# Optimization experiments

Measured on AMD Instinct MI355X. Metric: run time of the kernel, lower is better.

## Reference

```python
import jax, jax.numpy as jnp
import numpy as np

SOM_H, SOM_W = 16, 16
K = SOM_H * SOM_W          # num_embeddings = 256
EMB_D = 32                 # embedding_dim
ALPHA, BETA = 6.0, 1.0


def _build_tables():
    """Static SOM grid neighbor tables (rectangular geometry).
    ind[k] is a 0/1 row over the K codebook entries marking k and its
    up/down/left/right grid neighbors; counts[k] = number of neighbors incl self.
    Replaces the original per-voxel Python loop with a constant lookup table.
    """
    ind = np.zeros((K, K), np.float32)
    for idx in range(K):
        h, w = divmod(idx, SOM_W)
        neigh = [idx]
        if h - 1 >= 0:
            neigh.append((h - 1) * SOM_W + w)
        if h + 1 < SOM_H:
            neigh.append((h + 1) * SOM_W + w)
        if w - 1 >= 0:
            neigh.append(h * SOM_W + (w - 1))
        if w + 1 < SOM_W:
            neigh.append(h * SOM_W + (w + 1))
        ind[idx, neigh] = 1.0
    counts = ind.sum(axis=1)
    return jnp.asarray(ind), jnp.asarray(counts)

_IND_TABLE, _COUNTS = _build_tables()


def setup_inputs() -> dict:
    key = jax.random.key(0)
    k1, k2 = jax.random.split(key)
    x = jax.random.normal(k1, (8, EMB_D, 32, 32, 32), dtype=jnp.float32)  # [B,C,D,H,W]
    W = jax.random.normal(k2, (K, EMB_D), dtype=jnp.float32)              # codebook
    return {"x": x, "W": W}


def reference(x, W):
    # channels-last: [B, D, H, Wd, C]
    inputs = jnp.transpose(x, (0, 2, 3, 4, 1))
    in_shape = inputs.shape
    flat = inputs.reshape(-1, EMB_D)                    # [N, d]
    flat_sg = jax.lax.stop_gradient(flat)               # matches flat_inputs.detach()

    # squared Euclidean distances to all codebook entries: [N, K]
    dist = (jnp.sum(flat_sg ** 2, axis=1, keepdims=True)
            + jnp.sum(W ** 2, axis=1)
            - 2.0 * flat_sg @ W.T)

    enc_idx = jnp.argmin(dist, axis=1)                  # [N]
    encodings = jax.nn.one_hot(enc_idx, K, dtype=inputs.dtype)  # [N, K]

    quantized = (encodings @ W).reshape(in_shape)
    commitment_loss = jnp.mean((quantized - inputs) ** 2)

    # vectorized neighbor indicator + counts via static table gather
    indicator = _IND_TABLE[enc_idx]                     # [N, K], constant wrt floats
    total_neighbors = jnp.sum(_COUNTS[enc_idx])
    somloss = jnp.sum(dist * indicator) / total_neighbors

    loss = ALPHA * commitment_loss + BETA * somloss

    # straight-through estimator
    quantized_st = inputs + jax.lax.stop_gradient(quantized - inputs)
    out = jnp.transpose(quantized_st, (0, 4, 1, 2, 3))  # back to [B,C,D,H,W]
    return loss, out, encodings
```

## Files before the change

kernel.cpp:

```cpp
#include <hip/hip_runtime.h>


#define SOM_K      256
#define EMB_D      32
#define WPAD       36
#define N_VOX      262144
#define SPATIAL    32768
#define OUT_ELEMS  8388608
#define COMMIT_DEN 8388608.0f
#define NSLOT      256

__global__ __launch_bounds__(256) void som_prep_kernel(float* __restrict__ ws) {
  float4* p = (float4*)ws;
  int t = threadIdx.x;
#pragma unroll
  for (int i = 0; i < 4; ++i) p[i * 256 + t] = make_float4(0.f, 0.f, 0.f, 0.f);
}

__global__ __launch_bounds__(256) void som_main_kernel(
    const float* __restrict__ x,
    const float* __restrict__ w,
    float* __restrict__ slots,
    float* __restrict__ out,
    float* __restrict__ enc) {
  __shared__ __align__(16) float wl[SOM_K * WPAD];
  __shared__ float wsql[SOM_K];

  const int t = threadIdx.x;

  const int n    = blockIdx.x * 256 + t;
  const int base = (n >> 15) * (EMB_D * SPATIAL) + (n & (SPATIAL - 1));
  float xv[EMB_D];
#pragma unroll
  for (int c = 0; c < EMB_D; ++c) xv[c] = x[base + c * SPATIAL];

#pragma unroll
  for (int i = 0; i < 32; ++i) {
    int e = i * 256 + t;
    int r = e >> 5, c = e & 31;
    wl[r * WPAD + c] = w[e];
  }
  {
    float s = 0.0f;
#pragma unroll
    for (int c = 0; c < EMB_D; ++c) {
      float v = w[t * EMB_D + c];
      s = fmaf(v, v, s);
    }
    wsql[t] = s;
  }
  __syncthreads();

  float xsq = 0.0f;
#pragma unroll
  for (int c = 0; c < EMB_D; ++c) xsq = fmaf(xv[c], xv[c], xsq);

  float best = 3.402823466e38f;
  int   bidx = 0;
#pragma unroll 2
  for (int k = 0; k < SOM_K; ++k) {
    const float4* row = (const float4*)(wl + k * WPAD);
    float dot = 0.0f;
#pragma unroll
    for (int j = 0; j < 8; ++j) {
      float4 q = row[j];
      dot = fmaf(q.x, xv[4 * j + 0], dot);
      dot = fmaf(q.y, xv[4 * j + 1], dot);
      dot = fmaf(q.z, xv[4 * j + 2], dot);
      dot = fmaf(q.w, xv[4 * j + 3], dot);
    }
    float d = (xsq + wsql[k]) - 2.0f * dot;
    if (d < best) { best = d; bidx = k; }
  }

  {
    const int lane = t & 63, wave = t >> 6;
    float* ep = enc + (size_t)(blockIdx.x * 256 + wave * 64) * SOM_K + lane;
    const int c1 = lane + 64, c2 = lane + 128, c3 = lane + 192;
    for (int row = 0; row < 64; ++row) {
      const int src = __builtin_amdgcn_readlane(bidx, row);
      ep[0]   = (lane == src) ? 1.0f : 0.0f;
      ep[64]  = (c1   == src) ? 1.0f : 0.0f;
      ep[128] = (c2   == src) ? 1.0f : 0.0f;
      ep[192] = (c3   == src) ? 1.0f : 0.0f;
      ep += SOM_K;
    }
  }

  float commit = 0.0f;
  {
    const float4* qrow = (const float4*)(wl + bidx * WPAD);
#pragma unroll
    for (int j = 0; j < 8; ++j) {
      float4 q = qrow[j];
      float qq[4] = { q.x, q.y, q.z, q.w };
#pragma unroll
      for (int u = 0; u < 4; ++u) {
        int c = 4 * j + u;
        out[base + c * SPATIAL] = qq[u];
        float df = qq[u] - xv[c];
        commit = fmaf(df, df, commit);
      }
    }
  }

  float som = best;
  float cnt = 1.0f;
  {
    const int h  = bidx >> 4;
    const int wc = bidx & 15;
    const int   cand[4]  = { bidx - 16, bidx + 16, bidx - 1, bidx + 1 };
    const float valid[4] = { h > 0 ? 1.f : 0.f,  h < 15 ? 1.f : 0.f,
                             wc > 0 ? 1.f : 0.f, wc < 15 ? 1.f : 0.f };
#pragma unroll
    for (int j = 0; j < 4; ++j) {
      int nk = valid[j] != 0.0f ? cand[j] : bidx;
      const float4* nrow = (const float4*)(wl + nk * WPAD);
      float dot = 0.0f;
#pragma unroll
      for (int jj = 0; jj < 8; ++jj) {
        float4 q = nrow[jj];
        dot = fmaf(q.x, xv[4 * jj + 0], dot);
        dot = fmaf(q.y, xv[4 * jj + 1], dot);
        dot = fmaf(q.z, xv[4 * jj + 2], dot);
        dot = fmaf(q.w, xv[4 * jj + 3], dot);
      }
      float d = (xsq + wsql[nk]) - 2.0f * dot;
      som = fmaf(valid[j], d, som);
      cnt += valid[j];
    }
  }

  for (int off = 32; off > 0; off >>= 1) {
    commit += __shfl_down(commit, off, 64);
    som    += __shfl_down(som,    off, 64);
    cnt    += __shfl_down(cnt,    off, 64);
  }
  if ((t & 63) == 0) {
    float* sp = slots + (size_t)(blockIdx.x & (NSLOT - 1)) * 16;
    atomicAdd(sp + 0, commit);
    atomicAdd(sp + 1, som);
    atomicAdd(sp + 2, cnt);
  }
}

__global__ __launch_bounds__(64) void som_final_kernel(
    const float* __restrict__ slots, float* __restrict__ loss) {
  const int t = threadIdx.x;
  float commit = 0.f, som = 0.f, cnt = 0.f;
#pragma unroll
  for (int i = 0; i < 4; ++i) {
    const float* sp = slots + (size_t)(i * 64 + t) * 16;
    commit += sp[0]; som += sp[1]; cnt += sp[2];
  }
  for (int off = 32; off > 0; off >>= 1) {
    commit += __shfl_down(commit, off, 64);
    som    += __shfl_down(som,    off, 64);
    cnt    += __shfl_down(cnt,    off, 64);
  }
  if (t == 0) loss[0] = 6.0f * (commit / COMMIT_DEN) + som / cnt;
}

extern "C" void kernel_launch(void* const* d_in, const int* in_sizes, int n_in,
                              void* d_out, int out_size, void* d_ws, size_t ws_size,
                              hipStream_t stream) {
  const float* x = (const float*)d_in[0];
  const float* w = (const float*)d_in[1];
  float* ws  = (float*)d_ws;
  float* o   = (float*)d_out;

  som_prep_kernel<<<1, 256, 0, stream>>>(ws);
  som_main_kernel<<<N_VOX / 256, 256, 0, stream>>>(
      x, w, ws, o + 1, o + 1 + OUT_ELEMS);
  som_final_kernel<<<1, 64, 0, stream>>>(ws, o);
}
```

Measured before the change: 413.2 us.

## Split SOM kernel into argmin scan pass and separate write pass

```diff
diff --git a/kernel.cpp b/kernel.cpp
--- a/kernel.cpp
+++ b/kernel.cpp
@@ -17,12 +17,10 @@
   for (int i = 0; i < 4; ++i) p[i * 256 + t] = make_float4(0.f, 0.f, 0.f, 0.f);
 }
 
-__global__ __launch_bounds__(256) void som_main_kernel(
+__global__ __launch_bounds__(256) void som_scan_kernel(
     const float* __restrict__ x,
     const float* __restrict__ w,
-    float* __restrict__ slots,
-    float* __restrict__ out,
-    float* __restrict__ enc) {
+    int* __restrict__ bidx_out) {
   __shared__ __align__(16) float wl[SOM_K * WPAD];
   __shared__ float wsql[SOM_K];
 
@@ -73,12 +71,55 @@
     if (d < best) { best = d; bidx = k; }
   }
 
+  bidx_out[(size_t)n * SOM_K] = bidx;
+}
+
+__global__ __launch_bounds__(256) void som_write_kernel(
+    const float* __restrict__ x,
+    const float* __restrict__ w,
+    float* __restrict__ slots,
+    float* __restrict__ out,
+    float* enc) {
+  __shared__ __align__(16) float wl[SOM_K * WPAD];
+  __shared__ float wsql[SOM_K];
+
+  const int t = threadIdx.x;
+  const int n    = blockIdx.x * 256 + t;
+  const int base = (n >> 15) * (EMB_D * SPATIAL) + (n & (SPATIAL - 1));
+
+  const int mybidx = ((const int*)enc)[(size_t)n * SOM_K];
+
+  float xv[EMB_D];
+#pragma unroll
+  for (int c = 0; c < EMB_D; ++c) xv[c] = x[base + c * SPATIAL];
+
+#pragma unroll
+  for (int i = 0; i < 32; ++i) {
+    int e = i * 256 + t;
+    int r = e >> 5, c = e & 31;
+    wl[r * WPAD + c] = w[e];
+  }
+  {
+    float s = 0.0f;
+#pragma unroll
+    for (int c = 0; c < EMB_D; ++c) {
+      float v = w[t * EMB_D + c];
+      s = fmaf(v, v, s);
+    }
+    wsql[t] = s;
+  }
+  __syncthreads();
+
+  float xsq = 0.0f;
+#pragma unroll
+  for (int c = 0; c < EMB_D; ++c) xsq = fmaf(xv[c], xv[c], xsq);
+
   {
     const int lane = t & 63, wave = t >> 6;
     float* ep = enc + (size_t)(blockIdx.x * 256 + wave * 64) * SOM_K + lane;
     const int c1 = lane + 64, c2 = lane + 128, c3 = lane + 192;
     for (int row = 0; row < 64; ++row) {
-      const int src = __builtin_amdgcn_readlane(bidx, row);
+      const int src = __builtin_amdgcn_readlane(mybidx, row);
       ep[0]   = (lane == src) ? 1.0f : 0.0f;
       ep[64]  = (c1   == src) ? 1.0f : 0.0f;
       ep[128] = (c2   == src) ? 1.0f : 0.0f;
@@ -89,7 +130,7 @@
 
   float commit = 0.0f;
   {
-    const float4* qrow = (const float4*)(wl + bidx * WPAD);
+    const float4* qrow = (const float4*)(wl + mybidx * WPAD);
 #pragma unroll
     for (int j = 0; j < 8; ++j) {
       float4 q = qrow[j];
@@ -104,17 +145,29 @@
     }
   }
 
-  float som = best;
-  float cnt = 1.0f;
-  {
-    const int h  = bidx >> 4;
-    const int wc = bidx & 15;
-    const int   cand[4]  = { bidx - 16, bidx + 16, bidx - 1, bidx + 1 };
+  float som, cnt = 1.0f;
+  {
+    const float4* brow = (const float4*)(wl + mybidx * WPAD);
+    float dot = 0.0f;
+#pragma unroll
+    for (int j = 0; j < 8; ++j) {
+      float4 q = brow[j];
+      dot = fmaf(q.x, xv[4 * j + 0], dot);
+      dot = fmaf(q.y, xv[4 * j + 1], dot);
+      dot = fmaf(q.z, xv[4 * j + 2], dot);
+      dot = fmaf(q.w, xv[4 * j + 3], dot);
+    }
+    som = (xsq + wsql[mybidx]) - 2.0f * dot;
+  }
+  {
+    const int h  = mybidx >> 4;
+    const int wc = mybidx & 15;
+    const int   cand[4]  = { mybidx - 16, mybidx + 16, mybidx - 1, mybidx + 1 };
     const float valid[4] = { h > 0 ? 1.f : 0.f,  h < 15 ? 1.f : 0.f,
                              wc > 0 ? 1.f : 0.f, wc < 15 ? 1.f : 0.f };
 #pragma unroll
     for (int j = 0; j < 4; ++j) {
-      int nk = valid[j] != 0.0f ? cand[j] : bidx;
+      int nk = valid[j] != 0.0f ? cand[j] : mybidx;
       const float4* nrow = (const float4*)(wl + nk * WPAD);
       float dot = 0.0f;
 #pragma unroll
@@ -168,9 +221,10 @@
   const float* w = (const float*)d_in[1];
   float* ws  = (float*)d_ws;
   float* o   = (float*)d_out;
+  float* enc = o + 1 + OUT_ELEMS;
 
   som_prep_kernel<<<1, 256, 0, stream>>>(ws);
-  som_main_kernel<<<N_VOX / 256, 256, 0, stream>>>(
-      x, w, ws, o + 1, o + 1 + OUT_ELEMS);
+  som_scan_kernel<<<N_VOX / 256, 256, 0, stream>>>(x, w, (int*)enc);
+  som_write_kernel<<<N_VOX / 256, 256, 0, stream>>>(x, w, ws, o + 1, enc);
   som_final_kernel<<<1, 64, 0, stream>>>(ws, o);
 }
```

Result: slower. 442.8 us (+7.2%).

## Split one-hot encoding write into separate vectorized kernel

Applied to the files above, without the earlier changes.

```diff
diff --git a/kernel.cpp b/kernel.cpp
--- a/kernel.cpp
+++ b/kernel.cpp
@@ -17,7 +17,7 @@
   for (int i = 0; i < 4; ++i) p[i * 256 + t] = make_float4(0.f, 0.f, 0.f, 0.f);
 }
 
-__global__ __launch_bounds__(256) void som_main_kernel(
+__global__ __launch_bounds__(256) void som_scan_kernel(
     const float* __restrict__ x,
     const float* __restrict__ w,
     float* __restrict__ slots,
@@ -73,19 +73,7 @@
     if (d < best) { best = d; bidx = k; }
   }
 
-  {
-    const int lane = t & 63, wave = t >> 6;
-    float* ep = enc + (size_t)(blockIdx.x * 256 + wave * 64) * SOM_K + lane;
-    const int c1 = lane + 64, c2 = lane + 128, c3 = lane + 192;
-    for (int row = 0; row < 64; ++row) {
-      const int src = __builtin_amdgcn_readlane(bidx, row);
-      ep[0]   = (lane == src) ? 1.0f : 0.0f;
-      ep[64]  = (c1   == src) ? 1.0f : 0.0f;
-      ep[128] = (c2   == src) ? 1.0f : 0.0f;
-      ep[192] = (c3   == src) ? 1.0f : 0.0f;
-      ep += SOM_K;
-    }
-  }
+  ((int*)enc)[(size_t)n * SOM_K] = bidx;
 
   float commit = 0.0f;
   {
@@ -144,6 +132,33 @@
   }
 }
 
+__global__ __launch_bounds__(256) void som_enc_kernel(float* enc) {
+  const int t = threadIdx.x;
+  const int lane = t & 63, wave = t >> 6;
+  const size_t row0 = (size_t)blockIdx.x * 256 + (size_t)wave * 64;
+
+  const int myidx = ((const int*)enc)[(row0 + lane) * SOM_K];
+
+  float* rowp = enc + row0 * SOM_K;
+  for (int r = 0; r < 64; ++r) {
+    const int src = __builtin_amdgcn_readlane(myidx, r);
+    if (lane < 63) {
+      const int c0 = 3 + 4 * lane;
+      float4 v;
+      v.x = (c0     == src) ? 1.0f : 0.0f;
+      v.y = (c0 + 1 == src) ? 1.0f : 0.0f;
+      v.z = (c0 + 2 == src) ? 1.0f : 0.0f;
+      v.w = (c0 + 3 == src) ? 1.0f : 0.0f;
+      *(float4*)(rowp + 3 + 4 * lane) = v;
+    }
+    if (lane < 4) {
+      const int col = (lane == 3) ? 255 : lane;
+      rowp[col] = (col == src) ? 1.0f : 0.0f;
+    }
+    rowp += SOM_K;
+  }
+}
+
 __global__ __launch_bounds__(64) void som_final_kernel(
     const float* __restrict__ slots, float* __restrict__ loss) {
   const int t = threadIdx.x;
@@ -168,9 +183,10 @@
   const float* w = (const float*)d_in[1];
   float* ws  = (float*)d_ws;
   float* o   = (float*)d_out;
+  float* enc = o + 1 + OUT_ELEMS;
 
   som_prep_kernel<<<1, 256, 0, stream>>>(ws);
-  som_main_kernel<<<N_VOX / 256, 256, 0, stream>>>(
-      x, w, ws, o + 1, o + 1 + OUT_ELEMS);
+  som_scan_kernel<<<N_VOX / 256, 256, 0, stream>>>(x, w, ws, o + 1, enc);
+  som_enc_kernel<<<N_VOX / 256, 256, 0, stream>>>(enc);
   som_final_kernel<<<1, 64, 0, stream>>>(ws, o);
 }
```

Result: slower. 510.0 us (+23.4%).
